# Optimization experiments

Hardware: AMD Instinct MI355X
Metric: run time of the kernel (lower is better)

## Reference

```python
import jax, jax.numpy as jnp
import numpy as np
import math

NUM_HEADS = 16
TOPK = 64
EMBED = 1024

def setup_inputs() -> dict:
    key = jax.random.key(0)
    ks = jax.random.split(key, 11)
    b, s, e = 2, 2048, EMBED
    scale = 1.0 / math.sqrt(e)
    inp = {
        'q': jax.random.normal(ks[0], (b, s, e), dtype=jnp.float32),
        'k': jax.random.normal(ks[1], (b, s, e), dtype=jnp.float32),
        'v': jax.random.normal(ks[2], (b, s, e), dtype=jnp.float32),
        'Wq': jax.random.normal(ks[3], (e, e), dtype=jnp.float32) * scale,
        'bq': jnp.zeros((e,), dtype=jnp.float32),
        'Wk': jax.random.normal(ks[4], (e, e), dtype=jnp.float32) * scale,
        'bk': jnp.zeros((e,), dtype=jnp.float32),
        'Wv': jax.random.normal(ks[5], (e, e), dtype=jnp.float32) * scale,
        'bv': jnp.zeros((e,), dtype=jnp.float32),
        'Wo': jax.random.normal(ks[6], (e, e), dtype=jnp.float32) * scale,
        'bo': jnp.zeros((e,), dtype=jnp.float32),
    }
    return inp

def _topk_attention(Q, K, V, topk):
    # Q,K,V: (b, h, s, d)
    d = Q.shape[-1]
    scores = jnp.einsum('bhqd,bhkd->bhqk', Q, K) / jnp.sqrt(jnp.asarray(d, Q.dtype))
    topk_scores, topk_idx = jax.lax.top_k(scores, topk)  # (b,h,s,topk)
    probs = jax.nn.softmax(topk_scores, axis=-1)
    # gather V rows per (b,h): V_bh[idx] -> (s, topk, d); avoids (b,h,s,s,d) expand
    gather = jax.vmap(jax.vmap(lambda Vbh, idx: Vbh[idx]))
    sel = gather(V, topk_idx)  # (b,h,s,topk,d)
    return jnp.einsum('bhqk,bhqkd->bhqd', probs, sel)

def reference(q, k, v, Wq, bq, Wk, bk, Wv, bv, Wo, bo):
    b, s, e = q.shape
    h = NUM_HEADS
    d = e // h
    # NOTE: original torch code reshapes (b, s, e) -> (b, h, s, d) directly (no transpose)
    Q = (q @ Wq.T + bq).reshape(b, h, s, d)
    K = (k @ Wk.T + bk).reshape(b, h, s, d)
    V = (v @ Wv.T + bv).reshape(b, h, s, d)
    attn = _topk_attention(Q, K, V, TOPK)  # (b,h,s,d)
    out = attn.reshape(b, s, e)
    return out @ Wo.T + bo
```

## Files before the change

### kernel.cpp

```cpp
#include <hip/hip_runtime.h>
#include <stdint.h>

using u8  = unsigned char;
using s8  = signed char;
using u16 = unsigned short;
using u32 = unsigned int;
using u64 = unsigned long long;

typedef int   v4i __attribute__((ext_vector_type(4)));
typedef float v4f __attribute__((ext_vector_type(4)));
typedef short v8s __attribute__((ext_vector_type(8)));

__device__ __forceinline__ u16 f2bf(float f){
  u32 u = __builtin_bit_cast(u32, f);
  u32 r = (u + 0x7FFFu + ((u >> 16) & 1u)) >> 16;
  return (u16)r;
}
__device__ __forceinline__ float bf2f(u16 b){
  u32 u = ((u32)b) << 16;
  return __builtin_bit_cast(float, u);
}

__global__ __launch_bounds__(256) void quant_digits(
    const float* __restrict__ in, s8* __restrict__ dig, int n, float scale, float clampv)
{
  int t = blockIdx.x * 256 + threadIdx.x;
  int n8 = n >> 3;
  if (t >= n8) return;
  const float4* inv = (const float4*)in;
  float4 a = inv[2*t], b = inv[2*t+1];
  float xs[8] = {a.x,a.y,a.z,a.w,b.x,b.y,b.z,b.w};
  u64 p0=0,p1=0,p2=0,p3=0;
#pragma unroll
  for (int j=0;j<8;j++){
    float xv = fminf(fmaxf(xs[j], -clampv), clampv);
    int X = (int)rintf(xv * scale);
    int d0 = (int)(s8)(X & 255); X = (X - d0) >> 8;
    int d1 = (int)(s8)(X & 255); X = (X - d1) >> 8;
    int d2 = (int)(s8)(X & 255); X = (X - d2) >> 8;
    int d3 = X;
    p0 |= ((u64)(u8)(s8)d0) << (8*j);
    p1 |= ((u64)(u8)(s8)d1) << (8*j);
    p2 |= ((u64)(u8)(s8)d2) << (8*j);
    p3 |= ((u64)(u8)(s8)d3) << (8*j);
  }
  u64* o = (u64*)dig;
  size_t np8 = (size_t)n8;
  o[t] = p0; o[np8 + t] = p1; o[2*np8 + t] = p2; o[3*np8 + t] = p3;
}

#define MFMA_I8(c, a, b) asm volatile("v_mfma_i32_16x16x64_i8 %0, %1, %2, %0" : "+v"(c) : "v"(a), "v"(b))

__global__ __launch_bounds__(256) void gemm_i8(
    const s8* __restrict__ Ad, const s8* __restrict__ Wd, const float* __restrict__ bias,
    double* __restrict__ Cd, u16* __restrict__ Cb)
{
  __shared__ alignas(16) s8 As[4][32][80];
  __shared__ alignas(16) s8 Bs[4][32][80];
  const int i0 = blockIdx.x * 32, o0 = blockIdx.y * 32;
  const int t = threadIdx.x, w = t >> 6, lane = t & 63;
  const int wr = w >> 1, wc = w & 1, l15 = lane & 15, lg = lane >> 4;
  const size_t APL = 4194304, WPL = 1048576;

  v4i c0={0,0,0,0}, c1={0,0,0,0}, c2={0,0,0,0}, c3={0,0,0,0}, c4={0,0,0,0};

  for (int kt = 0; kt < 16; ++kt){
#pragma unroll
    for (int j = 0; j < 2; ++j){
      int cid = t*2 + j;
      int p = cid >> 7, rem = cid & 127;
      int row = rem >> 2, c16 = (rem & 3) << 4;
      int4 av = *(const int4*)(Ad + (size_t)p*APL + (size_t)(i0+row)*1024 + kt*64 + c16);
      *(int4*)&As[p][row][c16] = av;
      int4 bv = *(const int4*)(Wd + (size_t)p*WPL + (size_t)(o0+row)*1024 + kt*64 + c16);
      *(int4*)&Bs[p][row][c16] = bv;
    }
    __syncthreads();
    v4i a0 = *(const v4i*)&As[0][wr*16+l15][lg*16];
    v4i a1 = *(const v4i*)&As[1][wr*16+l15][lg*16];
    v4i a2 = *(const v4i*)&As[2][wr*16+l15][lg*16];
    v4i a3 = *(const v4i*)&As[3][wr*16+l15][lg*16];
    v4i b0 = *(const v4i*)&Bs[0][wc*16+l15][lg*16];
    v4i b1 = *(const v4i*)&Bs[1][wc*16+l15][lg*16];
    v4i b2 = *(const v4i*)&Bs[2][wc*16+l15][lg*16];
    v4i b3 = *(const v4i*)&Bs[3][wc*16+l15][lg*16];
    MFMA_I8(c0, a0, b2); MFMA_I8(c0, a1, b1); MFMA_I8(c0, a2, b0);
    MFMA_I8(c1, a0, b3); MFMA_I8(c1, a1, b2); MFMA_I8(c1, a2, b1); MFMA_I8(c1, a3, b0);
    MFMA_I8(c2, a1, b3); MFMA_I8(c2, a2, b2); MFMA_I8(c2, a3, b1);
    MFMA_I8(c3, a2, b3); MFMA_I8(c3, a3, b2);
    MFMA_I8(c4, a3, b3);
    __syncthreads();
  }
  const int oc = o0 + wc*16 + l15;
  const double bv = (double)bias[oc];
#pragma unroll
  for (int e = 0; e < 4; ++e){
    double val = (double)c0[e]*0x1p-43 + (double)c1[e]*0x1p-35 + (double)c2[e]*0x1p-27
               + (double)c3[e]*0x1p-19 + (double)c4[e]*0x1p-11 + bv;
    int orow = i0 + wr*16 + lg*4 + e;
    size_t idx = (size_t)orow*1024 + oc;
    Cd[idx] = val;
    Cb[idx] = f2bf((float)val);
  }
}

template<int ABF16, int OUTBF>
__global__ __launch_bounds__(256) void gemm_bf16k(
    const void* __restrict__ Ap, const float* __restrict__ W, const float* __restrict__ bias,
    void* __restrict__ C)
{
  __shared__ alignas(16) u16 As[32][72];
  __shared__ alignas(16) u16 Bs[32][72];
  const int i0 = blockIdx.x * 32, o0 = blockIdx.y * 32;
  const int t = threadIdx.x, w = t >> 6, lane = t & 63;
  const int wr = w >> 1, wc = w & 1, l15 = lane & 15, lg = lane >> 4;
  const int row = t >> 3, c8 = (t & 7) * 8;
  v4f acc = {0.f,0.f,0.f,0.f};
  for (int kt = 0; kt < 16; ++kt){
    if (ABF16){
      v8s x = *(const v8s*)((const u16*)Ap + (size_t)(i0+row)*1024 + kt*64 + c8);
      *(v8s*)&As[row][c8] = x;
    } else {
      const float* A = (const float*)Ap;
      const float4 x0 = *(const float4*)(A + (size_t)(i0+row)*1024 + kt*64 + c8);
      const float4 x1 = *(const float4*)(A + (size_t)(i0+row)*1024 + kt*64 + c8 + 4);
      v8s pk;
      pk[0]=(short)f2bf(x0.x); pk[1]=(short)f2bf(x0.y); pk[2]=(short)f2bf(x0.z); pk[3]=(short)f2bf(x0.w);
      pk[4]=(short)f2bf(x1.x); pk[5]=(short)f2bf(x1.y); pk[6]=(short)f2bf(x1.z); pk[7]=(short)f2bf(x1.w);
      *(v8s*)&As[row][c8] = pk;
    }
    {
      const float4 y0 = *(const float4*)(W + (size_t)(o0+row)*1024 + kt*64 + c8);
      const float4 y1 = *(const float4*)(W + (size_t)(o0+row)*1024 + kt*64 + c8 + 4);
      v8s pk;
      pk[0]=(short)f2bf(y0.x); pk[1]=(short)f2bf(y0.y); pk[2]=(short)f2bf(y0.z); pk[3]=(short)f2bf(y0.w);
      pk[4]=(short)f2bf(y1.x); pk[5]=(short)f2bf(y1.y); pk[6]=(short)f2bf(y1.z); pk[7]=(short)f2bf(y1.w);
      *(v8s*)&Bs[row][c8] = pk;
    }
    __syncthreads();
    v8s a0 = *(const v8s*)&As[wr*16+l15][lg*8];
    v8s a1 = *(const v8s*)&As[wr*16+l15][lg*8+32];
    v8s b0 = *(const v8s*)&Bs[wc*16+l15][lg*8];
    v8s b1 = *(const v8s*)&Bs[wc*16+l15][lg*8+32];
    acc = __builtin_amdgcn_mfma_f32_16x16x32_bf16(a0, b0, acc, 0, 0, 0);
    acc = __builtin_amdgcn_mfma_f32_16x16x32_bf16(a1, b1, acc, 0, 0, 0);
    __syncthreads();
  }
  const int oc = o0 + wc*16 + l15;
  const float bvv = bias[oc];
#pragma unroll
  for (int e=0;e<4;e++){
    int orow = i0 + wr*16 + lg*4 + e;
    size_t idx = (size_t)orow*1024 + oc;
    if (OUTBF) ((u16*)C)[idx] = f2bf(acc[e] + bvv);
    else       ((float*)C)[idx] = acc[e] + bvv;
  }
}

__global__ __launch_bounds__(512, 4) void attn_topk(
    const u16* __restrict__ Qb, const u16* __restrict__ Kb,
    const double* __restrict__ Qd, const double* __restrict__ Kd,
    const u16* __restrict__ Vb, u16* __restrict__ Ab, u32* __restrict__ flags)
{
  __shared__ u32 candL[32*256];
  __shared__ u64 selpL[16*64];
  __shared__ int cntA[32];

  const int lid = blockIdx.y * 64 + blockIdx.x;
  const int bh  = (lid & 7) * 4 + (lid >> 9);
  const int qb  = (lid >> 3) & 63;
  const size_t base = (size_t)(bh >> 4) * 2097152 + (size_t)(bh & 15) * 131072;
  const int q0 = qb * 32;
  const int tid = threadIdx.x, w = tid >> 6, lane = tid & 63;
  const int l15 = lane & 15, lg = lane >> 4;
  const u64 ltmask = (1ull << lane) - 1ull;

  if (tid < 32) cntA[tid] = 0;
  __syncthreads();

  const v4f vzero = {0.f,0.f,0.f,0.f};
  float nrmA, nrmB;
  {
    const size_t qoffA = base + (size_t)(q0 + l15)*64 + lg*8;
    v8s aA0 = *(const v8s*)(Qb + qoffA);
    v8s aA1 = *(const v8s*)(Qb + qoffA + 32);
    v8s aB0 = *(const v8s*)(Qb + qoffA + 1024);
    v8s aB1 = *(const v8s*)(Qb + qoffA + 1024 + 32);

    nrmA = 0.f; nrmB = 0.f;
#pragma unroll
    for (int m = 0; m < 8; ++m){
      float xA0 = bf2f((u16)aA0[m]), xA1 = bf2f((u16)aA1[m]);
      float xB0 = bf2f((u16)aB0[m]), xB1 = bf2f((u16)aB1[m]);
      nrmA = fmaf(xA0,xA0,nrmA); nrmA = fmaf(xA1,xA1,nrmA);
      nrmB = fmaf(xB0,xB0,nrmB); nrmB = fmaf(xB1,xB1,nrmB);
    }
    nrmA += __shfl_xor(nrmA,16); nrmA += __shfl_xor(nrmA,32);
    nrmB += __shfl_xor(nrmB,16); nrmB += __shfl_xor(nrmB,32);
    float T0A[4], T0B[4];
#pragma unroll
    for (int e = 0; e < 4; ++e){
      T0A[e] = 0.2f * sqrtf(__shfl(nrmA, lg*4 + e));
      T0B[e] = 0.2f * sqrtf(__shfl(nrmB, lg*4 + e));
    }

    const u16* Kw = Kb + base + (size_t)(w*256 + l15)*64 + lg*8;
    v8s b0 = *(const v8s*)(Kw);
    v8s b1 = *(const v8s*)(Kw + 32);

    auto step = [&](int kt, v8s b0c, v8s b1c){
      v4f sA = __builtin_amdgcn_mfma_f32_16x16x32_bf16(aA0, b0c, vzero, 0,0,0);
      sA = __builtin_amdgcn_mfma_f32_16x16x32_bf16(aA1, b1c, sA, 0,0,0);
      v4f sB = __builtin_amdgcn_mfma_f32_16x16x32_bf16(aB0, b0c, vzero, 0,0,0);
      sB = __builtin_amdgcn_mfma_f32_16x16x32_bf16(aB1, b1c, sB, 0,0,0);
      const u32 col = (u32)(w*256 + kt*16 + l15);
#pragma unroll
      for (int e = 0; e < 4; ++e){
        float sc = sA[e]*0.125f;
        if (sc >= T0A[e]){
          int row = lg*4 + e;
          int pos = atomicAdd(&cntA[row], 1);
          if (pos < 256) candL[row*256 + pos] = ((u32)f2bf(sc)<<16) | col;
        }
        float sc2 = sB[e]*0.125f;
        if (sc2 >= T0B[e]){
          int row = 16 + lg*4 + e;
          int pos = atomicAdd(&cntA[row], 1);
          if (pos < 256) candL[row*256 + pos] = ((u32)f2bf(sc2)<<16) | col;
        }
      }
    };

    for (int kt = 0; kt < 15; ++kt){
      v8s n0 = *(const v8s*)(Kw + (size_t)(kt+1)*1024);
      v8s n1 = *(const v8s*)(Kw + (size_t)(kt+1)*1024 + 32);
      step(kt, b0, b1);
      b0 = n0; b1 = n1;
    }
    step(15, b0, b1);
  }
  __syncthreads();

  for (int pass = 0; pass < 2; ++pass){
    const int R0 = pass*16 + w*2;
    const float nrmP0 = (pass == 0) ? nrmA : nrmB;
    u32 pk0[2], pk1[2], pk2[2], pk3[2], cstore[2], tv[2];
    bool fail[2];

#pragma unroll
    for (int rr = 0; rr < 2; ++rr){
      const int R = R0 + rr;
      int craw = cntA[R];
      fail[rr] = (craw > 256);
      cstore[rr] = (u32)(craw > 256 ? 256 : craw);
#pragma unroll
      for (int s = 0; s < 4; ++s){
        u32 idx = (u32)(64*s + lane);
        u32 val = (idx < cstore[rr]) ? candL[R*256 + idx] : 0u;
        if (s == 0) pk0[rr] = val; else if (s == 1) pk1[rr] = val;
        else if (s == 2) pk2[rr] = val; else pk3[rr] = val;
      }
      tv[rr] = 0u;
    }

    for (int bit = 14; bit >= 0; --bit){
#pragma unroll
      for (int rr = 0; rr < 2; ++rr){
        u32 tt = tv[rr] | (1u << bit);
        int c = (int)__popcll(__ballot((pk0[rr] >> 16) >= tt))
              + (int)__popcll(__ballot((pk1[rr] >> 16) >= tt))
              + (int)__popcll(__ballot((pk2[rr] >> 16) >= tt))
              + (int)__popcll(__ballot((pk3[rr] >> 16) >= tt));
        if (c >= 64) tv[rr] = tt;
      }
    }

    int na[2], nb[2];
#pragma unroll
    for (int rr = 0; rr < 2; ++rr){
      const int R = R0 + rr;
      const int Rl = R & 15;
      float t64f = bf2f((u16)tv[rr]);
      float T0R = 0.2f * sqrtf(__shfl(nrmP0, R & 15));
      float thi = t64f + 0.052f, tlo = t64f - 0.052f;
      int a_ = 0, b_ = 0;
#pragma unroll
      for (int s = 0; s < 4; ++s){
        u32 pkv = (s == 0) ? pk0[rr] : ((s == 1) ? pk1[rr] : ((s == 2) ? pk2[rr] : pk3[rr]));
        bool act = (u32)(64*s + lane) < cstore[rr];
        float v = bf2f((u16)(pkv >> 16));
        bool aut = act && (v > thi);
        bool ban = act && !aut && (v >= tlo);
        u64 ma = __ballot(aut);
        if (aut){
          int pos = a_ + (int)__popcll(ma & ltmask);
          if (pos < 64) selpL[Rl*64 + pos] = ((u64)(pkv & 0xFFFF0000u) << 32) | (u64)(pkv & 0x7FFu);
        }
        a_ += (int)__popcll(ma);
        u64 mb = __ballot(ban);
        if (ban){
          int pos = b_ + (int)__popcll(mb & ltmask);
          if (pos < 64) candL[R*256 + pos] = pkv;
        }
        b_ += (int)__popcll(mb);
      }
      bool fl = fail[rr] || (t64f < T0R + 0.055f) || (t64f >= 3.98f) || (b_ > 64);
      fail[rr] = fl;
      if (lane == 0) flags[bh*2048 + q0 + R] = fl ? 1u : 0u;
      na[rr] = fl ? 64 : (a_ > 64 ? 64 : a_);
      nb[rr] = fl ? 0  : b_;
    }
    asm volatile("s_waitcnt lgkmcnt(0)" ::: "memory");
    __builtin_amdgcn_sched_barrier(0);

    const double* Kdh = Kd + base;
    const double* Qdh = Qd + base + (size_t)q0*64;
    u32 bpk[2];
#pragma unroll
    for (int rr = 0; rr < 2; ++rr)
      bpk[rr] = (lane < nb[rr]) ? candL[(R0+rr)*256 + lane] : 0u;
    double ac0[2] = {0,0}, ac1[2] = {0,0};
#pragma unroll 4
    for (int j = 0; j < 32; ++j){
#pragma unroll
      for (int rr = 0; rr < 2; ++rr){
        double2 kv = ((const double2*)(Kdh + (size_t)(bpk[rr] & 0x7FFu)*64))[j];
        double2 qv = ((const double2*)(Qdh + (size_t)(R0+rr)*64))[j];
        ac0[rr] = fma(qv.x, kv.x, ac0[rr]);
        ac1[rr] = fma(qv.y, kv.y, ac1[rr]);
      }
    }
    double mv[2]; int mi[2];
#pragma unroll
    for (int rr = 0; rr < 2; ++rr){
      mv[rr] = (lane < nb[rr]) ? (ac0[rr] + ac1[rr]) : -1.0e300;
      mi[rr] = (lane < nb[rr]) ? (int)(bpk[rr] & 0x7FFu) : 0x7FFFFFFF;
    }
    int maxnb = nb[0] > nb[1] ? nb[0] : nb[1];
    int rank[2] = {0,0};
    for (int j = 0; j < maxnb; ++j){
#pragma unroll
      for (int rr = 0; rr < 2; ++rr){
        double ov = __shfl(mv[rr], j); int oi = __shfl(mi[rr], j);
        rank[rr] += (ov > mv[rr] || (ov == mv[rr] && oi < mi[rr])) ? 1 : 0;
      }
    }
#pragma unroll
    for (int rr = 0; rr < 2; ++rr){
      int need = 64 - na[rr]; if (need > nb[rr]) need = nb[rr];
      if (lane < nb[rr] && rank[rr] < need)
        selpL[((R0+rr) & 15)*64 + na[rr] + rank[rr]] =
            ((u64)(bpk[rr] & 0xFFFF0000u) << 32) | (u64)(bpk[rr] & 0x7FFu);
    }
    asm volatile("s_waitcnt lgkmcnt(0)" ::: "memory");
    __builtin_amdgcn_sched_barrier(0);

    u32 sidx[2]; float scv[2], pp[2];
#pragma unroll
    for (int rr = 0; rr < 2; ++rr){
      u64 pr = selpL[((R0+rr) & 15)*64 + lane];
      sidx[rr] = (u32)pr & 0x7FFu;
      scv[rr] = __builtin_bit_cast(float, (u32)(pr >> 32));
    }
#pragma unroll
    for (int rr = 0; rr < 2; ++rr){
      float mx = scv[rr];
#pragma unroll
      for (int off = 32; off; off >>= 1) mx = fmaxf(mx, __shfl_xor(mx, off));
      float p = expf(scv[rr] - mx);
      float Z = p;
#pragma unroll
      for (int off = 32; off; off >>= 1) Z += __shfl_xor(Z, off);
      pp[rr] = p / Z;
    }
#pragma unroll
    for (int rr = 0; rr < 2; ++rr)
      selpL[((R0+rr) & 15)*64 + lane] = ((u64)__builtin_bit_cast(u32, pp[rr]) << 32) | (u64)sidx[rr];
    asm volatile("s_waitcnt lgkmcnt(0)" ::: "memory");
    __builtin_amdgcn_sched_barrier(0);

    const int h = lane >> 5, dl = lane & 31;
    float u0[2] = {0,0}, u1[2] = {0,0};
#pragma unroll 4
    for (int j = 0; j < 64; j += 2){
#pragma unroll
      for (int rr = 0; rr < 2; ++rr){
        u64 pr = selpL[((R0+rr) & 15)*64 + j + h];
        float pv = __builtin_bit_cast(float, (u32)(pr >> 32));
        u32 vv = *(const u32*)(Vb + base + (size_t)((u32)pr & 0x7FFu)*64 + 2*dl);
        u0[rr] = fmaf(pv, bf2f((u16)(vv & 0xFFFFu)), u0[rr]);
        u1[rr] = fmaf(pv, bf2f((u16)(vv >> 16)),     u1[rr]);
      }
    }
#pragma unroll
    for (int rr = 0; rr < 2; ++rr){
      u0[rr] += __shfl_xor(u0[rr], 32);
      u1[rr] += __shfl_xor(u1[rr], 32);
    }
    if (lane < 32){
#pragma unroll
      for (int rr = 0; rr < 2; ++rr){
        u32 o = (u32)f2bf(u0[rr]) | ((u32)f2bf(u1[rr]) << 16);
        *(u32*)(Ab + base + (size_t)(q0 + R0 + rr)*64 + 2*dl) = o;
      }
    }
  }
}

__global__ __launch_bounds__(256) void attn_fallback(
    const u32* __restrict__ flags, const double* __restrict__ Qd,
    const double* __restrict__ Kd, const u16* __restrict__ Vb,
    u16* __restrict__ Ab)
{
  __shared__ double ktileL[4][16*64];
  __shared__ double valsL[2048];
  __shared__ double qlds[64];
  __shared__ double selvL[64];
  __shared__ int    seliL[64];
  __shared__ float  ppL[64];
  __shared__ float  ovL[4][64];
  __shared__ double redv[4];
  __shared__ int    redi[4];
  __shared__ double bcv;
  __shared__ int    bci;
  __shared__ u32    mskL;

  const int blk = blockIdx.x;
  const int tid = threadIdx.x, w = tid >> 6, lane = tid & 63;

  if (tid == 0){
    u32 m = 0;
    for (int i = 0; i < 16; ++i) m |= (flags[blk*16 + i] ? 1u : 0u) << i;
    mskL = m;
  }
  __syncthreads();
  const u32 msk = mskL;
  if (msk == 0u) return;

  for (int i = 0; i < 16; ++i){
    if (!((msk >> i) & 1u)) continue;
    const int g = blk*16 + i;
    const int bh = g >> 11, qrow = g & 2047;
    const size_t base = (size_t)(bh >> 4)*2097152 + (size_t)(bh & 15)*131072;
    if (tid < 64) qlds[tid] = Qd[base + (size_t)qrow*64 + tid];
    __syncthreads();

    double* ktw = ktileL[w];
    const int gg = lane >> 4, r = lane & 15;
    for (int t = 0; t < 32; ++t){
      const int k0 = w*512 + t*16;
#pragma unroll
      for (int r2 = 0; r2 < 16; ++r2)
        ktw[r2*64 + ((lane + r2) & 63)] = Kd[base + (size_t)(k0 + r2)*64 + lane];
      double p = 0.0;
#pragma unroll
      for (int dd = 0; dd < 16; ++dd){
        int d = gg*16 + dd;
        p = fma(qlds[d], ktw[r*64 + ((d + r) & 63)], p);
      }
      p += __shfl_xor(p, 16);
      p += __shfl_xor(p, 32);
      if (lane < 16) valsL[k0 + lane] = p * 0.125;
    }
    __syncthreads();

    double myv[8];
#pragma unroll
    for (int m2 = 0; m2 < 8; ++m2) myv[m2] = valsL[tid*8 + m2];

    double pvv = 1.0e300; int pii = -1;
    for (int step = 0; step < 64; ++step){
      double bv = -1.0e300; int bi = 0x7FFFFFFF;
#pragma unroll
      for (int m2 = 0; m2 < 8; ++m2){
        double vv = myv[m2]; int col = tid*8 + m2;
        bool after = (vv < pvv) || (vv == pvv && col > pii);
        bool bet = after && (vv > bv || (vv == bv && col < bi));
        bv = bet ? vv : bv; bi = bet ? col : bi;
      }
#pragma unroll
      for (int off = 32; off; off >>= 1){
        double ov = __shfl_xor(bv, off); int oi = __shfl_xor(bi, off);
        bool tk = (ov > bv) || (ov == bv && oi < bi);
        bv = tk ? ov : bv; bi = tk ? oi : bi;
      }
      if (lane == 0){ redv[w] = bv; redi[w] = bi; }
      __syncthreads();
      if (tid == 0){
        double fv = redv[0]; int fi = redi[0];
#pragma unroll
        for (int x = 1; x < 4; ++x){
          bool tk = (redv[x] > fv) || (redv[x] == fv && redi[x] < fi);
          fv = tk ? redv[x] : fv; fi = tk ? redi[x] : fi;
        }
        bcv = fv; bci = fi; selvL[step] = fv; seliL[step] = fi;
      }
      __syncthreads();
      pvv = bcv; pii = bci;
    }

    if (w == 0){
      float sc = (float)selvL[lane];
      float mx = sc;
#pragma unroll
      for (int off = 32; off; off >>= 1) mx = fmaxf(mx, __shfl_xor(mx, off));
      float p = expf(sc - mx);
      float Z = p;
#pragma unroll
      for (int off = 32; off; off >>= 1) Z += __shfl_xor(Z, off);
      ppL[lane] = p / Z;
    }
    __syncthreads();

    float o = 0.f;
#pragma unroll
    for (int j = 0; j < 16; ++j){
      int jj = w*16 + j;
      o = fmaf(ppL[jj], bf2f(Vb[base + (size_t)seliL[jj]*64 + lane]), o);
    }
    ovL[w][lane] = o;
    __syncthreads();
    if (w == 0){
      float oo = (ovL[0][lane] + ovL[1][lane]) + (ovL[2][lane] + ovL[3][lane]);
      Ab[base + (size_t)qrow*64 + lane] = f2bf(oo);
    }
    __syncthreads();
  }
}

extern "C" void kernel_launch(void* const* d_in, const int* in_sizes, int n_in,
                              void* d_out, int out_size, void* d_ws, size_t ws_size,
                              hipStream_t stream)
{
  (void)in_sizes; (void)n_in; (void)out_size; (void)ws_size;
  const float* q  = (const float*)d_in[0];
  const float* k  = (const float*)d_in[1];
  const float* v  = (const float*)d_in[2];
  const float* Wq = (const float*)d_in[3];
  const float* bq = (const float*)d_in[4];
  const float* Wk = (const float*)d_in[5];
  const float* bk = (const float*)d_in[6];
  const float* Wv = (const float*)d_in[7];
  const float* bv = (const float*)d_in[8];
  const float* Wo = (const float*)d_in[9];
  const float* bo = (const float*)d_in[10];

  char* ws = (char*)d_ws;
  const size_t MB = 1048576;
  double* Qd  = (double*)(ws);
  double* Kd  = (double*)(ws + 32*MB);
  u16*    Qb  = (u16*)  (ws + 64*MB);
  u16*    Kb  = (u16*)  (ws + 72*MB);
  u16*    Abf = (u16*)  (ws + 80*MB);
  s8*     dact= (s8*)   (ws + 88*MB);
  u16*    Vbf = (u16*)  (ws + 88*MB);
  s8*     dw  = (s8*)   (ws + 104*MB);
  u32*    flg = (u32*)  (ws + 104*MB);

  quant_digits<<<2048, 256, 0, stream>>>(q,  dact, 4194304, 134217728.0f, 7.75f);
  quant_digits<<<512,  256, 0, stream>>>(Wq, dw,   1048576, 4294967296.0f, 0.2495f);
  gemm_i8<<<dim3(128, 32), 256, 0, stream>>>(dact, dw, bq, Qd, Qb);
  quant_digits<<<2048, 256, 0, stream>>>(k,  dact, 4194304, 134217728.0f, 7.75f);
  quant_digits<<<512,  256, 0, stream>>>(Wk, dw,   1048576, 4294967296.0f, 0.2495f);
  gemm_i8<<<dim3(128, 32), 256, 0, stream>>>(dact, dw, bk, Kd, Kb);
  gemm_bf16k<0,1><<<dim3(128, 32), 256, 0, stream>>>(v, Wv, bv, Vbf);
  attn_topk<<<dim3(64, 32), 512, 0, stream>>>(Qb, Kb, Qd, Kd, Vbf, Abf, flg);
  attn_fallback<<<4096, 256, 0, stream>>>(flg, Qd, Kd, Vbf, Abf);
  gemm_bf16k<1,0><<<dim3(128, 32), 256, 0, stream>>>(Abf, Wo, bo, d_out);
}
```

Measured before the change: 668.7 us.

## Shrink attention candidate buffers, pack selections to u32, drop lowest int8 partial product

The int8 split-digit projection GEMM drops its lowest-order partial-product accumulator (c0, weighted 2^-43), which removes three MFMAs per k-step at a small cost in precision. In the top-k attention kernel the per-row candidate capacity goes from 256 to 192 and the selection buffer is packed as u32 instead of u64. This cuts LDS use, which may let more blocks fit per CU, and removes one ballot/popcount round per radix bit. The probability/index pairs for the V gather are now broadcast with register shuffles instead of a round trip through LDS. In exchange, rows with more than 192 candidates hit the failure/fallback path more often.

Measured after the change: 660.4 us. No clear change (-1.2%).

```diff
diff --git a/kernel.cpp b/kernel.cpp
--- a/kernel.cpp
+++ b/kernel.cpp
@@ -62,7 +62,7 @@
   const int wr = w >> 1, wc = w & 1, l15 = lane & 15, lg = lane >> 4;
   const size_t APL = 4194304, WPL = 1048576;
 
-  v4i c0={0,0,0,0}, c1={0,0,0,0}, c2={0,0,0,0}, c3={0,0,0,0}, c4={0,0,0,0};
+  v4i c1={0,0,0,0}, c2={0,0,0,0}, c3={0,0,0,0}, c4={0,0,0,0};
 
   for (int kt = 0; kt < 16; ++kt){
 #pragma unroll
@@ -84,7 +84,6 @@
     v4i b1 = *(const v4i*)&Bs[1][wc*16+l15][lg*16];
     v4i b2 = *(const v4i*)&Bs[2][wc*16+l15][lg*16];
     v4i b3 = *(const v4i*)&Bs[3][wc*16+l15][lg*16];
-    MFMA_I8(c0, a0, b2); MFMA_I8(c0, a1, b1); MFMA_I8(c0, a2, b0);
     MFMA_I8(c1, a0, b3); MFMA_I8(c1, a1, b2); MFMA_I8(c1, a2, b1); MFMA_I8(c1, a3, b0);
     MFMA_I8(c2, a1, b3); MFMA_I8(c2, a2, b2); MFMA_I8(c2, a3, b1);
     MFMA_I8(c3, a2, b3); MFMA_I8(c3, a3, b2);
@@ -95,7 +94,7 @@
   const double bv = (double)bias[oc];
 #pragma unroll
   for (int e = 0; e < 4; ++e){
-    double val = (double)c0[e]*0x1p-43 + (double)c1[e]*0x1p-35 + (double)c2[e]*0x1p-27
+    double val = (double)c1[e]*0x1p-35 + (double)c2[e]*0x1p-27
                + (double)c3[e]*0x1p-19 + (double)c4[e]*0x1p-11 + bv;
     int orow = i0 + wr*16 + lg*4 + e;
     size_t idx = (size_t)orow*1024 + oc;
@@ -157,13 +156,14 @@
   }
 }
 
+#define CCAP 192
 __global__ __launch_bounds__(512, 4) void attn_topk(
     const u16* __restrict__ Qb, const u16* __restrict__ Kb,
     const double* __restrict__ Qd, const double* __restrict__ Kd,
     const u16* __restrict__ Vb, u16* __restrict__ Ab, u32* __restrict__ flags)
 {
-  __shared__ u32 candL[32*256];
-  __shared__ u64 selpL[16*64];
+  __shared__ u32 candL[32*CCAP];
+  __shared__ u32 selpL[16*64];
   __shared__ int cntA[32];
 
   const int lid = blockIdx.y * 64 + blockIdx.x;
@@ -220,13 +220,13 @@
         if (sc >= T0A[e]){
           int row = lg*4 + e;
           int pos = atomicAdd(&cntA[row], 1);
-          if (pos < 256) candL[row*256 + pos] = ((u32)f2bf(sc)<<16) | col;
+          if (pos < CCAP) candL[row*CCAP + pos] = ((u32)f2bf(sc)<<16) | col;
         }
         float sc2 = sB[e]*0.125f;
         if (sc2 >= T0B[e]){
           int row = 16 + lg*4 + e;
           int pos = atomicAdd(&cntA[row], 1);
-          if (pos < 256) candL[row*256 + pos] = ((u32)f2bf(sc2)<<16) | col;
+          if (pos < CCAP) candL[row*CCAP + pos] = ((u32)f2bf(sc2)<<16) | col;
         }
       }
     };
@@ -244,21 +244,20 @@
   for (int pass = 0; pass < 2; ++pass){
     const int R0 = pass*16 + w*2;
     const float nrmP0 = (pass == 0) ? nrmA : nrmB;
-    u32 pk0[2], pk1[2], pk2[2], pk3[2], cstore[2], tv[2];
+    u32 pk0[2], pk1[2], pk2[2], cstore[2], tv[2];
     bool fail[2];
 
 #pragma unroll
     for (int rr = 0; rr < 2; ++rr){
       const int R = R0 + rr;
       int craw = cntA[R];
-      fail[rr] = (craw > 256);
-      cstore[rr] = (u32)(craw > 256 ? 256 : craw);
-#pragma unroll
-      for (int s = 0; s < 4; ++s){
+      fail[rr] = (craw > CCAP);
+      cstore[rr] = (u32)(craw > CCAP ? CCAP : craw);
+#pragma unroll
+      for (int s = 0; s < 3; ++s){
         u32 idx = (u32)(64*s + lane);
-        u32 val = (idx < cstore[rr]) ? candL[R*256 + idx] : 0u;
-        if (s == 0) pk0[rr] = val; else if (s == 1) pk1[rr] = val;
-        else if (s == 2) pk2[rr] = val; else pk3[rr] = val;
+        u32 val = (idx < cstore[rr]) ? candL[R*CCAP + idx] : 0u;
+        if (s == 0) pk0[rr] = val; else if (s == 1) pk1[rr] = val; else pk2[rr] = val;
       }
       tv[rr] = 0u;
     }
@@ -269,8 +268,7 @@
         u32 tt = tv[rr] | (1u << bit);
         int c = (int)__popcll(__ballot((pk0[rr] >> 16) >= tt))
               + (int)__popcll(__ballot((pk1[rr] >> 16) >= tt))
-              + (int)__popcll(__ballot((pk2[rr] >> 16) >= tt))
-              + (int)__popcll(__ballot((pk3[rr] >> 16) >= tt));
+              + (int)__popcll(__ballot((pk2[rr] >> 16) >= tt));
         if (c >= 64) tv[rr] = tt;
       }
     }
@@ -285,8 +283,8 @@
       float thi = t64f + 0.052f, tlo = t64f - 0.052f;
       int a_ = 0, b_ = 0;
 #pragma unroll
-      for (int s = 0; s < 4; ++s){
-        u32 pkv = (s == 0) ? pk0[rr] : ((s == 1) ? pk1[rr] : ((s == 2) ? pk2[rr] : pk3[rr]));
+      for (int s = 0; s < 3; ++s){
+        u32 pkv = (s == 0) ? pk0[rr] : ((s == 1) ? pk1[rr] : pk2[rr]);
         bool act = (u32)(64*s + lane) < cstore[rr];
         float v = bf2f((u16)(pkv >> 16));
         bool aut = act && (v > thi);
@@ -294,13 +292,13 @@
         u64 ma = __ballot(aut);
         if (aut){
           int pos = a_ + (int)__popcll(ma & ltmask);
-          if (pos < 64) selpL[Rl*64 + pos] = ((u64)(pkv & 0xFFFF0000u) << 32) | (u64)(pkv & 0x7FFu);
+          if (pos < 64) selpL[Rl*64 + pos] = pkv;
         }
         a_ += (int)__popcll(ma);
         u64 mb = __ballot(ban);
         if (ban){
           int pos = b_ + (int)__popcll(mb & ltmask);
-          if (pos < 64) candL[R*256 + pos] = pkv;
+          if (pos < 64) candL[R*CCAP + pos] = pkv;
         }
         b_ += (int)__popcll(mb);
       }
@@ -318,7 +316,7 @@
     u32 bpk[2];
 #pragma unroll
     for (int rr = 0; rr < 2; ++rr)
-      bpk[rr] = (lane < nb[rr]) ? candL[(R0+rr)*256 + lane] : 0u;
+      bpk[rr] = (lane < nb[rr]) ? candL[(R0+rr)*CCAP + lane] : 0u;
     double ac0[2] = {0,0}, ac1[2] = {0,0};
 #pragma unroll 4
     for (int j = 0; j < 32; ++j){
@@ -349,8 +347,7 @@
     for (int rr = 0; rr < 2; ++rr){
       int need = 64 - na[rr]; if (need > nb[rr]) need = nb[rr];
       if (lane < nb[rr] && rank[rr] < need)
-        selpL[((R0+rr) & 15)*64 + na[rr] + rank[rr]] =
-            ((u64)(bpk[rr] & 0xFFFF0000u) << 32) | (u64)(bpk[rr] & 0x7FFu);
+        selpL[((R0+rr) & 15)*64 + na[rr] + rank[rr]] = bpk[rr];
     }
     asm volatile("s_waitcnt lgkmcnt(0)" ::: "memory");
     __builtin_amdgcn_sched_barrier(0);
@@ -358,9 +355,9 @@
     u32 sidx[2]; float scv[2], pp[2];
 #pragma unroll
     for (int rr = 0; rr < 2; ++rr){
-      u64 pr = selpL[((R0+rr) & 15)*64 + lane];
-      sidx[rr] = (u32)pr & 0x7FFu;
-      scv[rr] = __builtin_bit_cast(float, (u32)(pr >> 32));
+      u32 pr = selpL[((R0+rr) & 15)*64 + lane];
+      sidx[rr] = pr & 0x7FFu;
+      scv[rr] = __builtin_bit_cast(float, pr & 0xFFFF0000u);
     }
 #pragma unroll
     for (int rr = 0; rr < 2; ++rr){
@@ -373,19 +370,18 @@
       for (int off = 32; off; off >>= 1) Z += __shfl_xor(Z, off);
       pp[rr] = p / Z;
     }
-#pragma unroll
-    for (int rr = 0; rr < 2; ++rr)
-      selpL[((R0+rr) & 15)*64 + lane] = ((u64)__builtin_bit_cast(u32, pp[rr]) << 32) | (u64)sidx[rr];
-    asm volatile("s_waitcnt lgkmcnt(0)" ::: "memory");
-    __builtin_amdgcn_sched_barrier(0);
+    u64 myp0 = ((u64)__builtin_bit_cast(u32, pp[0]) << 32) | (u64)sidx[0];
+    u64 myp1 = ((u64)__builtin_bit_cast(u32, pp[1]) << 32) | (u64)sidx[1];
 
     const int h = lane >> 5, dl = lane & 31;
     float u0[2] = {0,0}, u1[2] = {0,0};
 #pragma unroll 4
     for (int j = 0; j < 64; j += 2){
+      u64 pr0 = __shfl(myp0, j + h);
+      u64 pr1 = __shfl(myp1, j + h);
 #pragma unroll
       for (int rr = 0; rr < 2; ++rr){
-        u64 pr = selpL[((R0+rr) & 15)*64 + j + h];
+        u64 pr = (rr == 0) ? pr0 : pr1;
         float pv = __builtin_bit_cast(float, (u32)(pr >> 32));
         u32 vv = *(const u32*)(Vb + base + (size_t)((u32)pr & 0x7FFu)*64 + 2*dl);
         u0[rr] = fmaf(pv, bf2f((u16)(vv & 0xFFFFu)), u0[rr]);
```
